# Performance work log

Measured on AMD Instinct MI355X. Metric: run time of the kernel, lower is better.

Reference implementation:

```python
import jax, jax.numpy as jnp
import numpy as np

B, S, D, H = 2, 2048, 1024, 16
HD = D // H  # 64


def setup_inputs() -> dict:
    key = jax.random.key(0)
    ks = jax.random.split(key, 10)
    inp = {
        "queries": jax.random.normal(ks[0], (B, S, D), dtype=jnp.float32),
        "keys": jax.random.normal(ks[1], (B, S, D), dtype=jnp.float32),
        "values": jax.random.normal(ks[2], (B, S, D), dtype=jnp.float32),
        "attention_mask": jax.random.randint(ks[3], (B, S), 0, 2, dtype=jnp.int32),
        # Linear params (torch nn.Linear: y = x @ W.T + b), scaled like default init
        "Wq": jax.random.normal(ks[4], (D, D), dtype=jnp.float32) / np.sqrt(D),
        "bq": jnp.zeros((D,), dtype=jnp.float32),
        "Wk": jax.random.normal(ks[5], (D, D), dtype=jnp.float32) / np.sqrt(D),
        "bk": jnp.zeros((D,), dtype=jnp.float32),
        "Wv": jax.random.normal(ks[6], (D, D), dtype=jnp.float32) / np.sqrt(D),
        "bv": jnp.zeros((D,), dtype=jnp.float32),
    }
    return inp


def _split_heads(x):
    # torch.chunk along last dim + stack(dim=1) == reshape + transpose
    b, s, d = x.shape
    return x.reshape(b, s, H, HD).transpose(0, 2, 1, 3)  # [B,H,S,hd]


def reference(queries, keys, values, attention_mask, Wq, bq, Wk, bk, Wv, bv):
    q = jax.nn.relu(queries @ Wq.T + bq)
    k = jax.nn.relu(keys @ Wk.T + bk)
    v = jax.nn.relu(values @ Wv.T + bv)
    qh, kh, vh = _split_heads(q), _split_heads(k), _split_heads(v)
    score = jnp.einsum("bhqd,bhkd->bhqk", qh, kh) / jnp.sqrt(jnp.float32(HD))
    # enc mask: [B,1,S,1] broadcast over key dim — masks whole query rows where mask==0
    row_mask = (attention_mask == 0)[:, None, :, None]
    score = jnp.where(row_mask, jnp.float32(-1e9), score)
    attn = jax.nn.softmax(score, axis=-1)
    a = jnp.einsum("bhqk,bhkd->bhqd", attn, vh)  # [B,H,S,hd]
    # faithful to original: permute(0,1,3,2) then reshape to (B,S,D)
    a = a.transpose(0, 1, 3, 2).reshape(q.shape[0], q.shape[1], q.shape[2])
    return a + queries
```

## Files before the change

kernel.cpp:

```cpp
#include <hip/hip_runtime.h>
#include <hip/hip_bf16.h>

#define DEV __device__ __forceinline__

typedef __attribute__((ext_vector_type(8))) short short8;
typedef __attribute__((ext_vector_type(4))) float f32x4;

#define MFMA16(a, b, c) __builtin_amdgcn_mfma_f32_16x16x32_bf16((a), (b), (c), 0, 0, 0)

static constexpr int B_ = 2, S_ = 2048, D_ = 1024, H_ = 16, HD_ = 64;
static constexpr long NX = (long)B_ * S_ * D_;
static constexpr long NW = (long)D_ * D_;

DEV short f2bf(float f) {
    __hip_bfloat16 h = __float2bfloat16(f);
    union { __hip_bfloat16 hh; short s; } u;
    u.hh = h;
    return u.s;
}

DEV float bf2f(short s) {
    union { float f; unsigned u; } x;
    x.u = ((unsigned)(unsigned short)s) << 16;
    return x.f;
}

DEV short8 ld8(const short* p) { return *(const short8*)p; }

DEV void gld16(const short* g, short* l) {
    __builtin_amdgcn_global_load_lds(
        (const __attribute__((address_space(1))) unsigned int*)g,
        (__attribute__((address_space(3))) unsigned int*)l, 16, 0, 0);
}

__global__ __launch_bounds__(256) void convert_all(
    const float* __restrict__ q, const float* __restrict__ k, const float* __restrict__ v,
    const float* __restrict__ wq, const float* __restrict__ wk, const float* __restrict__ wv,
    short* __restrict__ qb, short* __restrict__ kb, short* __restrict__ vb,
    short* __restrict__ wqb, short* __restrict__ wkb, short* __restrict__ wvb) {
    long tid = (long)blockIdx.x * 256 + threadIdx.x;
    long e = tid * 4;
    const float* src; short* dst; long off;
    if      (e < NX)            { src = q;  dst = qb;  off = e; }
    else if (e < 2*NX)          { src = k;  dst = kb;  off = e - NX; }
    else if (e < 3*NX)          { src = v;  dst = vb;  off = e - 2*NX; }
    else if (e < 3*NX + NW)     { src = wq; dst = wqb; off = e - 3*NX; }
    else if (e < 3*NX + 2*NW)   { src = wk; dst = wkb; off = e - 3*NX - NW; }
    else                        { src = wv; dst = wvb; off = e - 3*NX - 2*NW; }
    float4 f = *(const float4*)(src + off);
    short4 o;
    o.x = f2bf(f.x); o.y = f2bf(f.y); o.z = f2bf(f.z); o.w = f2bf(f.w);
    *(short4*)(dst + off) = o;
}

__global__ __launch_bounds__(256) void gemm_bias_relu(
    const short* __restrict__ X0, const short* __restrict__ X1, const short* __restrict__ X2,
    const short* __restrict__ W0, const short* __restrict__ W1, const short* __restrict__ W2,
    const float* __restrict__ b0, const float* __restrict__ b1, const float* __restrict__ b2,
    short* __restrict__ O0, short* __restrict__ O1, short* __restrict__ O2) {
    __shared__ short As[128 * 32];
    __shared__ short Bs[128 * 32];

    const int z = blockIdx.z;
    const short* X   = (z == 0) ? X0 : (z == 1) ? X1 : X2;
    const short* W   = (z == 0) ? W0 : (z == 1) ? W1 : W2;
    const float* bia = (z == 0) ? b0 : (z == 1) ? b1 : b2;
    short*       Out = (z == 0) ? O0 : (z == 1) ? O1 : O2;

    const int tid  = threadIdx.x;
    const int wid  = tid >> 6;
    const int lane = tid & 63;
    const int id   = lane & 15;
    const int quad = lane >> 4;
    const int m0 = blockIdx.y * 128;
    const int n0 = blockIdx.x * 128;
    const int wm = (wid >> 1) * 64;
    const int wn = (wid & 1) * 64;

    const short* Ag0 = X + (long)(m0 + wid * 32 + (lane >> 2)) * D_ + (lane & 3) * 8;
    const short* Bg0 = W + (long)(n0 + wid * 32 + (lane >> 2)) * D_ + (lane & 3) * 8;
    short* AsW0 = As + (wid * 32) * 32;
    short* AsW1 = As + (wid * 32 + 16) * 32;
    short* BsW0 = Bs + (wid * 32) * 32;
    short* BsW1 = Bs + (wid * 32 + 16) * 32;

    f32x4 acc[4][4] = {};

    for (int kk = 0; kk < D_; kk += 32) {
        __syncthreads();
        gld16(Ag0 + kk,            AsW0);
        gld16(Ag0 + 16 * D_ + kk,  AsW1);
        gld16(Bg0 + kk,            BsW0);
        gld16(Bg0 + 16 * D_ + kk,  BsW1);
        __syncthreads();

        short8 af[4], bf[4];
#pragma unroll
        for (int i = 0; i < 4; i++) af[i] = ld8(&As[(wm + 16*i + id) * 32 + quad * 8]);
#pragma unroll
        for (int j = 0; j < 4; j++) bf[j] = ld8(&Bs[(wn + 16*j + id) * 32 + quad * 8]);
#pragma unroll
        for (int i = 0; i < 4; i++)
#pragma unroll
            for (int j = 0; j < 4; j++)
                acc[i][j] = MFMA16(af[i], bf[j], acc[i][j]);
    }

#pragma unroll
    for (int j = 0; j < 4; j++) {
        int col = n0 + wn + 16*j + id;
        float bj = bia[col];
#pragma unroll
        for (int i = 0; i < 4; i++) {
#pragma unroll
            for (int r = 0; r < 4; r++) {
                int row = m0 + wm + 16*i + quad*4 + r;
                float val = fmaxf(acc[i][j][r] + bj, 0.f);
                Out[(long)row * D_ + col] = f2bf(val);
            }
        }
    }
}

__global__ __launch_bounds__(256) void transpose_v(const short* __restrict__ Vp,
                                                   short* __restrict__ VT) {
    __shared__ short tile[64][80];
    const int bh = blockIdx.y;
    const int b = bh >> 4, h = bh & 15;
    const int s0 = blockIdx.x * 64;
    const int t = threadIdx.x;
#pragma unroll
    for (int it = 0; it < 2; it++) {
        int row = (t >> 3) + 32 * it;
        int c8  = (t & 7) * 8;
        short8 d = ld8(Vp + (long)(b * S_ + s0 + row) * D_ + h * HD_ + c8);
        *(short8*)(&tile[row][c8]) = d;
    }
    __syncthreads();
#pragma unroll
    for (int it = 0; it < 2; it++) {
        int e = (t >> 3) + 32 * it;
        int sb = (t & 7) * 8;
        short8 o;
#pragma unroll
        for (int u = 0; u < 8; u++) o[u] = tile[sb + u][e];
        *(short8*)(VT + ((long)bh * HD_ + e) * S_ + s0 + sb) = o;
    }
}

__global__ __launch_bounds__(256, 2) void attention(
    const short* __restrict__ Qb, const short* __restrict__ Kb,
    const short* __restrict__ VT, const int* __restrict__ mask,
    const float* __restrict__ queries, float* __restrict__ out) {
    __shared__ short Ks[64 * 64];
    __shared__ short Vs[64 * 64];
    __shared__ short pl[4 * 2 * 16 * 72];

    const int tid  = threadIdx.x;
    const int wid  = tid >> 6;
    const int lane = tid & 63;
    const int id   = lane & 15;
    const int quad = lane >> 4;

    const int bid = blockIdx.x;
    const int qb_ = bid & 15;
    const int h   = (bid >> 4) & 15;
    const int b   = bid >> 8;
    const int q0  = qb_ * 128 + wid * 32;

    short8 qf[2][2];
#pragma unroll
    for (int g = 0; g < 2; g++) {
        const short* qbase = Qb + (long)(b * S_ + q0 + g * 16 + id) * D_ + h * HD_ + quad * 8;
        short8 f0 = ld8(qbase);
        short8 f1 = ld8(qbase + 32);
        const float qsc = mask[b * S_ + q0 + g * 16 + id] ? 0.125f : 0.f;
#pragma unroll
        for (int i = 0; i < 8; i++) {
            f0[i] = f2bf(bf2f(f0[i]) * qsc);
            f1[i] = f2bf(bf2f(f1[i]) * qsc);
        }
        qf[g][0] = f0; qf[g][1] = f1;
    }

    const int srow = wid * 16 + (lane >> 3);
    const int su   = (lane & 7) ^ (srow & 7);
    const short* kg0 = Kb + ((long)b * S_ + srow) * D_ + h * HD_ + su * 8;
    const short* vg0 = VT + (((long)(b * H_ + h) * HD_) + srow) * S_ + su * 8;
    short* KsW = Ks + wid * 1024;
    short* VsW = Vs + wid * 1024;
    short* plw = pl + wid * (2 * 16 * 72);

    const int swz = id & 7;

    float l4[2][4] = {};
    f32x4 o[2][4] = {};

    for (int c0 = 0; c0 < S_; c0 += 64) {
        __syncthreads();
        gld16(kg0 + (long)c0 * D_,            KsW);
        gld16(kg0 + (long)c0 * D_ + 8 * D_,   KsW + 512);
        gld16(vg0 + c0,                       VsW);
        gld16(vg0 + c0 + 8 * S_,              VsW + 512);
        __syncthreads();

        f32x4 s[2][4];
#pragma unroll
        for (int g = 0; g < 2; g++)
#pragma unroll
            for (int t = 0; t < 4; t++) s[g][t] = (f32x4){0.f, 0.f, 0.f, 0.f};
#pragma unroll
        for (int t = 0; t < 4; t++) {
            short8 a0 = ld8(&Ks[(16*t + id) * 64 + ((quad     ) ^ swz) * 8]);
            short8 a1 = ld8(&Ks[(16*t + id) * 64 + ((quad ^ 4 ) ^ swz) * 8]);
            s[0][t] = MFMA16(a0, qf[0][0], s[0][t]);
            s[0][t] = MFMA16(a1, qf[0][1], s[0][t]);
            s[1][t] = MFMA16(a0, qf[1][0], s[1][t]);
            s[1][t] = MFMA16(a1, qf[1][1], s[1][t]);
        }

#pragma unroll
        for (int g = 0; g < 2; g++) {
            short* plg = plw + g * (16 * 72);
#pragma unroll
            for (int t = 0; t < 4; t++) {
                float p0 = __expf(s[g][t][0]);
                float p1 = __expf(s[g][t][1]);
                float p2 = __expf(s[g][t][2]);
                float p3 = __expf(s[g][t][3]);
                l4[g][0] += p0; l4[g][1] += p1; l4[g][2] += p2; l4[g][3] += p3;
                short4 w4;
                w4.x = f2bf(p0); w4.y = f2bf(p1); w4.z = f2bf(p2); w4.w = f2bf(p3);
                *(short4*)(&plg[id * 72 + 16 * t + quad * 4]) = w4;
            }
        }
        short8 pf[2][2];
#pragma unroll
        for (int g = 0; g < 2; g++) {
            short* plg = plw + g * (16 * 72);
            pf[g][0] = ld8(&plg[id * 72 + quad * 8]);
            pf[g][1] = ld8(&plg[id * 72 + 32 + quad * 8]);
        }

#pragma unroll
        for (int j2 = 0; j2 < 4; j2++) {
#pragma unroll
            for (int kh = 0; kh < 2; kh++) {
                short8 va = ld8(&Vs[(16*j2 + id) * 64 + (((kh << 2) + quad) ^ swz) * 8]);
                o[0][j2] = MFMA16(va, pf[0][kh], o[0][j2]);
                o[1][j2] = MFMA16(va, pf[1][kh], o[1][j2]);
            }
        }
    }

    const long obase = (long)b * (S_ * D_) + (long)h * (HD_ * S_);
#pragma unroll
    for (int g = 0; g < 2; g++) {
        float l = l4[g][0] + l4[g][1] + l4[g][2] + l4[g][3];
        l += __shfl_xor(l, 16);
        l += __shfl_xor(l, 32);
        const float linv = 1.f / l;
#pragma unroll
        for (int j2 = 0; j2 < 4; j2++) {
#pragma unroll
            for (int r = 0; r < 4; r++) {
                int dim = 16 * j2 + quad * 4 + r;
                long idx = obase + (long)dim * S_ + q0 + g * 16 + id;
                out[idx] = o[g][j2][r] * linv + queries[idx];
            }
        }
    }
}

extern "C" void kernel_launch(void* const* d_in, const int* in_sizes, int n_in,
                              void* d_out, int out_size, void* d_ws, size_t ws_size,
                              hipStream_t stream) {
    const float* queries = (const float*)d_in[0];
    const float* keys    = (const float*)d_in[1];
    const float* values  = (const float*)d_in[2];
    const int*   mask    = (const int*)d_in[3];
    const float* Wq = (const float*)d_in[4];
    const float* bq = (const float*)d_in[5];
    const float* Wk = (const float*)d_in[6];
    const float* bk = (const float*)d_in[7];
    const float* Wv = (const float*)d_in[8];
    const float* bv = (const float*)d_in[9];
    float* out = (float*)d_out;

    short* ws  = (short*)d_ws;
    short* qb  = ws;
    short* kb  = qb  + NX;
    short* vb  = kb  + NX;
    short* wqb = vb  + NX;
    short* wkb = wqb + NW;
    short* wvb = wkb + NW;
    short* Q   = wvb + NW;
    short* K   = Q   + NX;
    short* Vp  = K   + NX;
    short* VT  = Vp  + NX;

    convert_all<<<15360, 256, 0, stream>>>(queries, keys, values, Wq, Wk, Wv,
                                           qb, kb, vb, wqb, wkb, wvb);
    gemm_bias_relu<<<dim3(8, 32, 3), 256, 0, stream>>>(qb, kb, vb, wqb, wkb, wvb,
                                                       bq, bk, bv, Q, K, Vp);
    transpose_v<<<dim3(32, 32), 256, 0, stream>>>(Vp, VT);
    attention<<<512, 256, 0, stream>>>(Q, K, VT, mask, queries, out);
}
```

Measured before the change: 207.5 us.

## Double-buffer LDS tiles in projection GEMM and attention, swizzle V transpose tile

The projection GEMM and the attention kernel now keep two LDS buffers. Each iteration issues the global-to-LDS load for the next K-slice or key/value chunk before computing on the current one, which removes one barrier per iteration and overlaps load latency with MFMA work. The V transpose drops its padded tile and uses an XOR-swizzled 64-wide layout to avoid LDS bank conflicts. The cost is twice the LDS for the GEMM and attention tiles, which could lower occupancy, and the code now relies on the barrier waiting for the previous iteration's async loads.

```diff
diff --git a/kernel.cpp b/kernel.cpp
--- a/kernel.cpp
+++ b/kernel.cpp
@@ -58,8 +58,8 @@
     const short* __restrict__ W0, const short* __restrict__ W1, const short* __restrict__ W2,
     const float* __restrict__ b0, const float* __restrict__ b1, const float* __restrict__ b2,
     short* __restrict__ O0, short* __restrict__ O1, short* __restrict__ O2) {
-    __shared__ short As[128 * 32];
-    __shared__ short Bs[128 * 32];
+    __shared__ short As[2][128 * 32];
+    __shared__ short Bs[2][128 * 32];
 
     const int z = blockIdx.z;
     const short* X   = (z == 0) ? X0 : (z == 1) ? X1 : X2;
@@ -79,26 +79,31 @@
 
     const short* Ag0 = X + (long)(m0 + wid * 32 + (lane >> 2)) * D_ + (lane & 3) * 8;
     const short* Bg0 = W + (long)(n0 + wid * 32 + (lane >> 2)) * D_ + (lane & 3) * 8;
-    short* AsW0 = As + (wid * 32) * 32;
-    short* AsW1 = As + (wid * 32 + 16) * 32;
-    short* BsW0 = Bs + (wid * 32) * 32;
-    short* BsW1 = Bs + (wid * 32 + 16) * 32;
+    const int offW = wid * 1024;
 
     f32x4 acc[4][4] = {};
 
+    gld16(Ag0,            &As[0][offW]);
+    gld16(Ag0 + 16 * D_,  &As[0][offW + 512]);
+    gld16(Bg0,            &Bs[0][offW]);
+    gld16(Bg0 + 16 * D_,  &Bs[0][offW + 512]);
+
     for (int kk = 0; kk < D_; kk += 32) {
+        const int cur = (kk >> 5) & 1;
         __syncthreads();
-        gld16(Ag0 + kk,            AsW0);
-        gld16(Ag0 + 16 * D_ + kk,  AsW1);
-        gld16(Bg0 + kk,            BsW0);
-        gld16(Bg0 + 16 * D_ + kk,  BsW1);
-        __syncthreads();
+        if (kk + 32 < D_) {
+            const int nxt = cur ^ 1;
+            gld16(Ag0 + kk + 32,            &As[nxt][offW]);
+            gld16(Ag0 + 16 * D_ + kk + 32,  &As[nxt][offW + 512]);
+            gld16(Bg0 + kk + 32,            &Bs[nxt][offW]);
+            gld16(Bg0 + 16 * D_ + kk + 32,  &Bs[nxt][offW + 512]);
+        }
 
         short8 af[4], bf[4];
 #pragma unroll
-        for (int i = 0; i < 4; i++) af[i] = ld8(&As[(wm + 16*i + id) * 32 + quad * 8]);
-#pragma unroll
-        for (int j = 0; j < 4; j++) bf[j] = ld8(&Bs[(wn + 16*j + id) * 32 + quad * 8]);
+        for (int i = 0; i < 4; i++) af[i] = ld8(&As[cur][(wm + 16*i + id) * 32 + quad * 8]);
+#pragma unroll
+        for (int j = 0; j < 4; j++) bf[j] = ld8(&Bs[cur][(wn + 16*j + id) * 32 + quad * 8]);
 #pragma unroll
         for (int i = 0; i < 4; i++)
 #pragma unroll
@@ -124,7 +129,7 @@
 
 __global__ __launch_bounds__(256) void transpose_v(const short* __restrict__ Vp,
                                                    short* __restrict__ VT) {
-    __shared__ short tile[64][80];
+    __shared__ short tile[64 * 64];
     const int bh = blockIdx.y;
     const int b = bh >> 4, h = bh & 15;
     const int s0 = blockIdx.x * 64;
@@ -132,18 +137,21 @@
 #pragma unroll
     for (int it = 0; it < 2; it++) {
         int row = (t >> 3) + 32 * it;
-        int c8  = (t & 7) * 8;
-        short8 d = ld8(Vp + (long)(b * S_ + s0 + row) * D_ + h * HD_ + c8);
-        *(short8*)(&tile[row][c8]) = d;
+        int u   = t & 7;
+        short8 d = ld8(Vp + (long)(b * S_ + s0 + row) * D_ + h * HD_ + u * 8);
+        *(short8*)(&tile[row * 64 + (u ^ ((row >> 3) & 7)) * 8]) = d;
     }
     __syncthreads();
 #pragma unroll
     for (int it = 0; it < 2; it++) {
-        int e = (t >> 3) + 32 * it;
+        int e  = (t >> 3) + 32 * it;
         int sb = (t & 7) * 8;
         short8 o;
 #pragma unroll
-        for (int u = 0; u < 8; u++) o[u] = tile[sb + u][e];
+        for (int u = 0; u < 8; u++) {
+            int row = sb + u;
+            o[u] = tile[row * 64 + (((e >> 3) ^ ((row >> 3) & 7)) * 8) + (e & 7)];
+        }
         *(short8*)(VT + ((long)bh * HD_ + e) * S_ + s0 + sb) = o;
     }
 }
@@ -152,9 +160,9 @@
     const short* __restrict__ Qb, const short* __restrict__ Kb,
     const short* __restrict__ VT, const int* __restrict__ mask,
     const float* __restrict__ queries, float* __restrict__ out) {
-    __shared__ short Ks[64 * 64];
-    __shared__ short Vs[64 * 64];
-    __shared__ short pl[4 * 2 * 16 * 72];
+    __shared__ short Ks[2][64 * 64];
+    __shared__ short Vs[2][64 * 64];
+    __shared__ short pl[4][2 * 16 * 72];
 
     const int tid  = threadIdx.x;
     const int wid  = tid >> 6;
@@ -187,22 +195,29 @@
     const int su   = (lane & 7) ^ (srow & 7);
     const short* kg0 = Kb + ((long)b * S_ + srow) * D_ + h * HD_ + su * 8;
     const short* vg0 = VT + (((long)(b * H_ + h) * HD_) + srow) * S_ + su * 8;
-    short* KsW = Ks + wid * 1024;
-    short* VsW = Vs + wid * 1024;
-    short* plw = pl + wid * (2 * 16 * 72);
+    short* plw = pl[wid];
 
     const int swz = id & 7;
 
     float l4[2][4] = {};
     f32x4 o[2][4] = {};
 
+    gld16(kg0,            &Ks[0][wid * 1024]);
+    gld16(kg0 + 8 * D_,   &Ks[0][wid * 1024 + 512]);
+    gld16(vg0,            &Vs[0][wid * 1024]);
+    gld16(vg0 + 8 * S_,   &Vs[0][wid * 1024 + 512]);
+
     for (int c0 = 0; c0 < S_; c0 += 64) {
+        const int cur = (c0 >> 6) & 1;
         __syncthreads();
-        gld16(kg0 + (long)c0 * D_,            KsW);
-        gld16(kg0 + (long)c0 * D_ + 8 * D_,   KsW + 512);
-        gld16(vg0 + c0,                       VsW);
-        gld16(vg0 + c0 + 8 * S_,              VsW + 512);
-        __syncthreads();
+        if (c0 + 64 < S_) {
+            const int nxt = cur ^ 1;
+            const long cg = (long)(c0 + 64);
+            gld16(kg0 + cg * D_,           &Ks[nxt][wid * 1024]);
+            gld16(kg0 + cg * D_ + 8 * D_,  &Ks[nxt][wid * 1024 + 512]);
+            gld16(vg0 + cg,                &Vs[nxt][wid * 1024]);
+            gld16(vg0 + cg + 8 * S_,       &Vs[nxt][wid * 1024 + 512]);
+        }
 
         f32x4 s[2][4];
 #pragma unroll
@@ -211,8 +226,8 @@
             for (int t = 0; t < 4; t++) s[g][t] = (f32x4){0.f, 0.f, 0.f, 0.f};
 #pragma unroll
         for (int t = 0; t < 4; t++) {
-            short8 a0 = ld8(&Ks[(16*t + id) * 64 + ((quad     ) ^ swz) * 8]);
-            short8 a1 = ld8(&Ks[(16*t + id) * 64 + ((quad ^ 4 ) ^ swz) * 8]);
+            short8 a0 = ld8(&Ks[cur][(16*t + id) * 64 + ((quad    ) ^ swz) * 8]);
+            short8 a1 = ld8(&Ks[cur][(16*t + id) * 64 + ((quad ^ 4) ^ swz) * 8]);
             s[0][t] = MFMA16(a0, qf[0][0], s[0][t]);
             s[0][t] = MFMA16(a1, qf[0][1], s[0][t]);
             s[1][t] = MFMA16(a0, qf[1][0], s[1][t]);
@@ -246,7 +261,7 @@
         for (int j2 = 0; j2 < 4; j2++) {
 #pragma unroll
             for (int kh = 0; kh < 2; kh++) {
-                short8 va = ld8(&Vs[(16*j2 + id) * 64 + (((kh << 2) + quad) ^ swz) * 8]);
+                short8 va = ld8(&Vs[cur][(16*j2 + id) * 64 + (((kh << 2) + quad) ^ swz) * 8]);
                 o[0][j2] = MFMA16(va, pf[0][kh], o[0][j2]);
                 o[1][j2] = MFMA16(va, pf[1][kh], o[1][j2]);
             }
```

Result: no change. 206.8 us (-0.4%).
